# Kernel tuning notes

Hardware: AMD Instinct MI355X
Metric: run time of the kernel (lower is better)

## Reference

```python
import jax, jax.numpy as jnp
import numpy as np

NUM_GRAPHS = 64


def _gcn_conv(x, src, dst, W, b, n_nodes):
    # PyG GCNConv: add self-loops, symmetric degree normalization, scatter-add.
    s = jnp.concatenate([src, jnp.arange(n_nodes, dtype=src.dtype)])
    d = jnp.concatenate([dst, jnp.arange(n_nodes, dtype=dst.dtype)])
    deg = jax.ops.segment_sum(jnp.ones_like(d, dtype=x.dtype), d, num_segments=n_nodes)
    dinv = jnp.where(deg > 0, jax.lax.rsqrt(deg), 0.0)
    h = x @ W  # transform before gather: [N, H]
    msg = (dinv[s] * dinv[d])[:, None] * h[s]  # [E+N, H]
    out = jax.ops.segment_sum(msg, d, num_segments=n_nodes)
    return out + b


def reference(x, edge_index, batch, W1, b1, W2, b2, fcW1, fcb1, fcW2, fcb2):
    n_nodes = x.shape[0]
    src, dst = edge_index[0], edge_index[1]
    h = jax.nn.relu(_gcn_conv(x, src, dst, W1, b1, n_nodes))
    # dropout(p=0.5, training=False) is identity at inference
    h = jax.nn.relu(_gcn_conv(h, src, dst, W2, b2, n_nodes))
    # global_mean_pool over graph ids
    sums = jax.ops.segment_sum(h, batch, num_segments=NUM_GRAPHS)
    cnts = jax.ops.segment_sum(jnp.ones((n_nodes,), dtype=h.dtype), batch, num_segments=NUM_GRAPHS)
    g = sums / jnp.maximum(cnts, 1.0)[:, None]  # [G, H]
    g = jax.nn.relu(g @ fcW1 + fcb1)
    logits = g @ fcW2 + fcb2
    return jax.nn.log_softmax(logits, axis=1)


def setup_inputs() -> dict:
    key = jax.random.key(0)
    ks = jax.random.split(key, 8)
    N, E, D, H, C = 100000, 1600000, 128, 128, 10
    x = jax.random.normal(ks[0], (N, D), dtype=jnp.float32)
    edge_index = jax.random.randint(ks[1], (2, E), 0, N, dtype=jnp.int32)
    batch = jnp.sort(jax.random.randint(ks[2], (N,), 0, NUM_GRAPHS, dtype=jnp.int32))
    def w(k, fan_in, shape):
        return jax.random.normal(k, shape, dtype=jnp.float32) / np.sqrt(fan_in)
    return {
        'x': x, 'edge_index': edge_index, 'batch': batch,
        'W1': w(ks[3], D, (D, H)), 'b1': jnp.zeros((H,), jnp.float32),
        'W2': w(ks[4], H, (H, H)), 'b2': jnp.zeros((H,), jnp.float32),
        'fcW1': w(ks[5], H, (H, H)), 'fcb1': jnp.zeros((H,), jnp.float32),
        'fcW2': w(ks[6], H, (H, C)), 'fcb2': jnp.zeros((C,), jnp.float32),
    }
```

## Files before the change

kernel.cpp:

```cpp
#include <hip/hip_runtime.h>
#include <stdint.h>

#define TB 256

__device__ __forceinline__ float blo(uint32_t v) { return __uint_as_float(v << 16); }
__device__ __forceinline__ float bhi(uint32_t v) { return __uint_as_float(v & 0xffff0000u); }
__device__ __forceinline__ uint32_t f2b(float f) {
    uint32_t u = __float_as_uint(f);
    return (u + 0x7fffu + ((u >> 16) & 1u)) >> 16;
}
__device__ __forceinline__ uint32_t pack2(float lo, float hi) {
    return f2b(lo) | (f2b(hi) << 16);
}

__global__ void zero_u32(uint32_t* __restrict__ p, int n) {
    int i = blockIdx.x * blockDim.x + threadIdx.x;
    if (i < n) p[i] = 0u;
}

__global__ void hist_kernel(const int* __restrict__ dst, int E, int* __restrict__ cnt) {
    int e = blockIdx.x * blockDim.x + threadIdx.x;
    if (e < E) atomicAdd(&cnt[dst[e]], 1);
}

__global__ void dinv_kernel(const int* __restrict__ cnt, float* __restrict__ dinv, int N) {
    int n = blockIdx.x * blockDim.x + threadIdx.x;
    if (n < N) dinv[n] = rsqrtf((float)cnt[n] + 1.0f);
}

__global__ __launch_bounds__(256) void scan1_kernel(const int* __restrict__ cnt, int N,
                                                    int* __restrict__ rp, int* __restrict__ bsum) {
    __shared__ int sh[256];
    int t = threadIdx.x;
    int base = blockIdx.x * 1024 + t * 4;
    int v0 = (base + 0 < N) ? cnt[base + 0] : 0;
    int v1 = (base + 1 < N) ? cnt[base + 1] : 0;
    int v2 = (base + 2 < N) ? cnt[base + 2] : 0;
    int v3 = (base + 3 < N) ? cnt[base + 3] : 0;
    int s = v0 + v1 + v2 + v3;
    sh[t] = s;
    __syncthreads();
    for (int off = 1; off < 256; off <<= 1) {
        int add = (t >= off) ? sh[t - off] : 0;
        __syncthreads();
        sh[t] += add;
        __syncthreads();
    }
    int incl = sh[t];
    if (t == 255) bsum[blockIdx.x] = incl;
    int run = incl - s;
    if (base + 0 < N) rp[base + 0] = run; run += v0;
    if (base + 1 < N) rp[base + 1] = run; run += v1;
    if (base + 2 < N) rp[base + 2] = run; run += v2;
    if (base + 3 < N) rp[base + 3] = run;
}

__global__ __launch_bounds__(256) void scan2_kernel(int* __restrict__ bsum, int nblk) {
    __shared__ int sh[256];
    int t = threadIdx.x;
    int v = (t < nblk) ? bsum[t] : 0;
    sh[t] = v;
    __syncthreads();
    for (int off = 1; off < 256; off <<= 1) {
        int add = (t >= off) ? sh[t - off] : 0;
        __syncthreads();
        sh[t] += add;
        __syncthreads();
    }
    if (t < nblk) bsum[t] = sh[t] - v;
}

__global__ void scan3_kernel(int* __restrict__ rp, int* __restrict__ rfill,
                             const int* __restrict__ bsum, int N, int E) {
    int i = blockIdx.x * blockDim.x + threadIdx.x;
    if (i < N) {
        int v = rp[i] + bsum[i >> 10];
        rp[i] = v;
        rfill[i] = v;
    }
    if (i == 0) rp[N] = E;
}

__global__ void fill_kernel(const int* __restrict__ src, const int* __restrict__ dst, int E,
                            int* __restrict__ rfill, int2* __restrict__ edges,
                            const float* __restrict__ dinv) {
    int e = blockIdx.x * blockDim.x + threadIdx.x;
    if (e < E) {
        int s = src[e], d = dst[e];
        int pos = atomicAdd(&rfill[d], 1);
        int2 pr;
        pr.x = s;
        pr.y = __float_as_int(dinv[s] * dinv[d]);
        edges[pos] = pr;
    }
}

template <bool BF16IN>
__global__ __launch_bounds__(256) void gemm128_kernel(const void* __restrict__ Xv,
                                                      const float* __restrict__ W,
                                                      uint32_t* __restrict__ Y,
                                                      int N, int ntiles) {
    __shared__ float Ws[128 * 128];
    for (int i = threadIdx.x; i < 128 * 128 / 4; i += 256)
        ((float4*)Ws)[i] = ((const float4*)W)[i];
    __syncthreads();

    int tf = threadIdx.x & 31;
    int tn = threadIdx.x >> 5;
    int f0 = tf * 4;
    int j0 = tn * 4;

    for (int tile = blockIdx.x; tile < ntiles; tile += gridDim.x) {
        int n0 = tile * 32;
        int nn0 = min(n0 + j0 + 0, N - 1);
        int nn1 = min(n0 + j0 + 1, N - 1);
        int nn2 = min(n0 + j0 + 2, N - 1);
        int nn3 = min(n0 + j0 + 3, N - 1);
        float4 a0 = {0, 0, 0, 0}, a1 = {0, 0, 0, 0}, a2 = {0, 0, 0, 0}, a3 = {0, 0, 0, 0};

        if (BF16IN) {
            const uint16_t* xr0 = (const uint16_t*)Xv + (size_t)nn0 * 128;
            const uint16_t* xr1 = (const uint16_t*)Xv + (size_t)nn1 * 128;
            const uint16_t* xr2 = (const uint16_t*)Xv + (size_t)nn2 * 128;
            const uint16_t* xr3 = (const uint16_t*)Xv + (size_t)nn3 * 128;
#pragma unroll 4
            for (int k = 0; k < 128; k += 2) {
                float4 w0 = *(const float4*)(Ws + k * 128 + f0);
                float4 w1 = *(const float4*)(Ws + (k + 1) * 128 + f0);
                uint32_t u0 = *(const uint32_t*)(xr0 + k);
                uint32_t u1 = *(const uint32_t*)(xr1 + k);
                uint32_t u2 = *(const uint32_t*)(xr2 + k);
                uint32_t u3 = *(const uint32_t*)(xr3 + k);
                float x;
                x = blo(u0);
                a0.x = fmaf(x, w0.x, a0.x); a0.y = fmaf(x, w0.y, a0.y);
                a0.z = fmaf(x, w0.z, a0.z); a0.w = fmaf(x, w0.w, a0.w);
                x = bhi(u0);
                a0.x = fmaf(x, w1.x, a0.x); a0.y = fmaf(x, w1.y, a0.y);
                a0.z = fmaf(x, w1.z, a0.z); a0.w = fmaf(x, w1.w, a0.w);
                x = blo(u1);
                a1.x = fmaf(x, w0.x, a1.x); a1.y = fmaf(x, w0.y, a1.y);
                a1.z = fmaf(x, w0.z, a1.z); a1.w = fmaf(x, w0.w, a1.w);
                x = bhi(u1);
                a1.x = fmaf(x, w1.x, a1.x); a1.y = fmaf(x, w1.y, a1.y);
                a1.z = fmaf(x, w1.z, a1.z); a1.w = fmaf(x, w1.w, a1.w);
                x = blo(u2);
                a2.x = fmaf(x, w0.x, a2.x); a2.y = fmaf(x, w0.y, a2.y);
                a2.z = fmaf(x, w0.z, a2.z); a2.w = fmaf(x, w0.w, a2.w);
                x = bhi(u2);
                a2.x = fmaf(x, w1.x, a2.x); a2.y = fmaf(x, w1.y, a2.y);
                a2.z = fmaf(x, w1.z, a2.z); a2.w = fmaf(x, w1.w, a2.w);
                x = blo(u3);
                a3.x = fmaf(x, w0.x, a3.x); a3.y = fmaf(x, w0.y, a3.y);
                a3.z = fmaf(x, w0.z, a3.z); a3.w = fmaf(x, w0.w, a3.w);
                x = bhi(u3);
                a3.x = fmaf(x, w1.x, a3.x); a3.y = fmaf(x, w1.y, a3.y);
                a3.z = fmaf(x, w1.z, a3.z); a3.w = fmaf(x, w1.w, a3.w);
            }
        } else {
            const float* xr0 = (const float*)Xv + (size_t)nn0 * 128;
            const float* xr1 = (const float*)Xv + (size_t)nn1 * 128;
            const float* xr2 = (const float*)Xv + (size_t)nn2 * 128;
            const float* xr3 = (const float*)Xv + (size_t)nn3 * 128;
#pragma unroll 8
            for (int k = 0; k < 128; ++k) {
                float4 wv = *(const float4*)(Ws + k * 128 + f0);
                float x0 = xr0[k], x1 = xr1[k], x2 = xr2[k], x3 = xr3[k];
                a0.x = fmaf(x0, wv.x, a0.x); a0.y = fmaf(x0, wv.y, a0.y);
                a0.z = fmaf(x0, wv.z, a0.z); a0.w = fmaf(x0, wv.w, a0.w);
                a1.x = fmaf(x1, wv.x, a1.x); a1.y = fmaf(x1, wv.y, a1.y);
                a1.z = fmaf(x1, wv.z, a1.z); a1.w = fmaf(x1, wv.w, a1.w);
                a2.x = fmaf(x2, wv.x, a2.x); a2.y = fmaf(x2, wv.y, a2.y);
                a2.z = fmaf(x2, wv.z, a2.z); a2.w = fmaf(x2, wv.w, a2.w);
                a3.x = fmaf(x3, wv.x, a3.x); a3.y = fmaf(x3, wv.y, a3.y);
                a3.z = fmaf(x3, wv.z, a3.z); a3.w = fmaf(x3, wv.w, a3.w);
            }
        }
        int n;
        n = n0 + j0 + 0;
        if (n < N) { uint2 o = {pack2(a0.x, a0.y), pack2(a0.z, a0.w)};
                     *(uint2*)(Y + (size_t)n * 64 + tf * 2) = o; }
        n = n0 + j0 + 1;
        if (n < N) { uint2 o = {pack2(a1.x, a1.y), pack2(a1.z, a1.w)};
                     *(uint2*)(Y + (size_t)n * 64 + tf * 2) = o; }
        n = n0 + j0 + 2;
        if (n < N) { uint2 o = {pack2(a2.x, a2.y), pack2(a2.z, a2.w)};
                     *(uint2*)(Y + (size_t)n * 64 + tf * 2) = o; }
        n = n0 + j0 + 3;
        if (n < N) { uint2 o = {pack2(a3.x, a3.y), pack2(a3.z, a3.w)};
                     *(uint2*)(Y + (size_t)n * 64 + tf * 2) = o; }
    }
}

__global__ __launch_bounds__(256) void conv_kernel(const uint32_t* __restrict__ T,
                                                   const int* __restrict__ rp,
                                                   const int2* __restrict__ edges,
                                                   const float* __restrict__ dinv,
                                                   const float* __restrict__ bias,
                                                   uint32_t* __restrict__ OUT, int N) {
    int wid = (blockIdx.x * TB + threadIdx.x) >> 6;
    int lane = threadIdx.x & 63;
    if (wid >= N) return;
    int d = wid;
    float dv = dinv[d];
    uint32_t td = T[(size_t)d * 64 + lane];
    float accx = dv * dv * blo(td);
    float accy = dv * dv * bhi(td);
    int e0 = rp[d], e1 = rp[d + 1];
#pragma unroll 4
    for (int e = e0; e < e1; ++e) {
        int2 pr = edges[e];
        float w = __int_as_float(pr.y);
        uint32_t tv = T[(size_t)pr.x * 64 + lane];
        accx = fmaf(w, blo(tv), accx);
        accy = fmaf(w, bhi(tv), accy);
    }
    float2 b = *(const float2*)(bias + lane * 2);
    OUT[(size_t)d * 64 + lane] = pack2(fmaxf(accx + b.x, 0.0f), fmaxf(accy + b.y, 0.0f));
}

#define NPB 256
__global__ __launch_bounds__(128) void pool_kernel(const uint16_t* __restrict__ Hh,
                                                   const int* __restrict__ batch, int N,
                                                   float* __restrict__ gsum, int* __restrict__ gcnt) {
    int f = threadIdx.x;
    int n0 = blockIdx.x * NPB;
    if (n0 >= N) return;
    int n1 = min(n0 + NPB, N);
    int cur = batch[n0];
    float acc = 0.0f;
    int c = 0;
    for (int n = n0; n < n1; ++n) {
        int b = batch[n];
        if (b != cur) {
            atomicAdd(&gsum[cur * 128 + f], acc);
            if (f == 0) atomicAdd(&gcnt[cur], c);
            acc = 0.0f; c = 0; cur = b;
        }
        acc += __uint_as_float(((uint32_t)Hh[(size_t)n * 128 + f]) << 16);
        c++;
    }
    atomicAdd(&gsum[cur * 128 + f], acc);
    if (f == 0) atomicAdd(&gcnt[cur], c);
}

__global__ __launch_bounds__(128) void head_kernel(const float* __restrict__ gsum,
                                                   const int* __restrict__ gcnt,
                                                   const float* __restrict__ fcW1,
                                                   const float* __restrict__ fcb1,
                                                   const float* __restrict__ fcW2,
                                                   const float* __restrict__ fcb2,
                                                   float* __restrict__ out) {
    __shared__ float gx[128], hid[128], lg[10];
    int g = blockIdx.x, t = threadIdx.x;
    float cntf = fmaxf((float)gcnt[g], 1.0f);
    gx[t] = gsum[g * 128 + t] / cntf;
    __syncthreads();
    float a = fcb1[t];
    for (int k = 0; k < 128; ++k) a = fmaf(gx[k], fcW1[k * 128 + t], a);
    hid[t] = fmaxf(a, 0.0f);
    __syncthreads();
    if (t < 10) {
        float a2 = fcb2[t];
        for (int k = 0; k < 128; ++k) a2 = fmaf(hid[k], fcW2[k * 10 + t], a2);
        lg[t] = a2;
    }
    __syncthreads();
    if (t < 10) {
        float m = -1e30f;
        for (int j = 0; j < 10; ++j) m = fmaxf(m, lg[j]);
        float se = 0.0f;
        for (int j = 0; j < 10; ++j) se += expf(lg[j] - m);
        out[g * 10 + t] = lg[t] - m - logf(se);
    }
}

extern "C" void kernel_launch(void* const* d_in, const int* in_sizes, int n_in,
                              void* d_out, int out_size, void* d_ws, size_t ws_size,
                              hipStream_t stream) {
    const float* x    = (const float*)d_in[0];
    const int*   ei   = (const int*)d_in[1];
    const int*   batch= (const int*)d_in[2];
    const float* W1   = (const float*)d_in[3];
    const float* b1   = (const float*)d_in[4];
    const float* W2   = (const float*)d_in[5];
    const float* b2   = (const float*)d_in[6];
    const float* fcW1 = (const float*)d_in[7];
    const float* fcb1 = (const float*)d_in[8];
    const float* fcW2 = (const float*)d_in[9];
    const float* fcb2 = (const float*)d_in[10];
    float* out = (float*)d_out;

    int N = in_sizes[0] / 128;
    int E = in_sizes[1] / 2;
    const int* src = ei;
    const int* dst = ei + E;

    char* basep = (char*)d_ws;
    size_t off = 0;
    auto alloc = [&](size_t bytes) -> void* {
        off = (off + 255) & ~(size_t)255;
        void* p = basep + off;
        off += bytes;
        return p;
    };
    float*     dinv  = (float*)alloc((size_t)N * 4);
    int*       cnt   = (int*)alloc((size_t)N * 4);
    int*       rp    = (int*)alloc((size_t)(N + 1) * 4);
    int*       rfill = (int*)alloc((size_t)N * 4);
    int*       bsum  = (int*)alloc(1024 * 4);
    int2*      edges = (int2*)alloc((size_t)E * 8);
    uint32_t*  A     = (uint32_t*)alloc((size_t)N * 128 * 2);
    uint32_t*  B     = (uint32_t*)alloc((size_t)N * 128 * 2);
    float*     gsum  = (float*)alloc(64 * 128 * 4);
    int*       gcnt  = (int*)alloc(64 * 4);

    int nblk = (N + 1023) / 1024;
    int ntiles = (N + 31) / 32;

    zero_u32<<<(N + TB - 1) / TB, TB, 0, stream>>>((uint32_t*)cnt, N);
    hist_kernel<<<(E + TB - 1) / TB, TB, 0, stream>>>(dst, E, cnt);
    dinv_kernel<<<(N + TB - 1) / TB, TB, 0, stream>>>(cnt, dinv, N);

    scan1_kernel<<<nblk, 256, 0, stream>>>(cnt, N, rp, bsum);
    scan2_kernel<<<1, 256, 0, stream>>>(bsum, nblk);
    scan3_kernel<<<(N + TB - 1) / TB, TB, 0, stream>>>(rp, rfill, bsum, N, E);
    fill_kernel<<<(E + TB - 1) / TB, TB, 0, stream>>>(src, dst, E, rfill, edges, dinv);

    gemm128_kernel<false><<<1024, 256, 0, stream>>>(x, W1, A, N, ntiles);
    conv_kernel<<<(N + 3) / 4, TB, 0, stream>>>(A, rp, edges, dinv, b1, B, N);

    gemm128_kernel<true><<<1024, 256, 0, stream>>>(B, W2, A, N, ntiles);
    conv_kernel<<<(N + 3) / 4, TB, 0, stream>>>(A, rp, edges, dinv, b2, B, N);

    zero_u32<<<(64 * 128 + TB - 1) / TB, TB, 0, stream>>>((uint32_t*)gsum, 64 * 128);
    zero_u32<<<1, 64, 0, stream>>>((uint32_t*)gcnt, 64);
    pool_kernel<<<(N + NPB - 1) / NPB, 128, 0, stream>>>((const uint16_t*)B, batch, N, gsum, gcnt);

    head_kernel<<<64, 128, 0, stream>>>(gsum, gcnt, fcW1, fcb1, fcW2, fcb2, out);
}
```

Baseline: 628.1 us.

## Replace scalar FMA node-transform GEMM with bf16 MFMA kernel

Replaces the FP32 FMA-based 128x128 GEMM with a kernel using MFMA 16x16x32 bf16 instructions. Weights are converted to bf16 and stored transposed in padded shared memory, then held in registers as B fragments. The fp32 input for layer one is rounded to bf16 before the multiply, which adds precision loss in exchange for higher matrix throughput. Output is written as scattered 16-bit stores.

```diff
diff --git a/kernel.cpp b/kernel.cpp
--- a/kernel.cpp
+++ b/kernel.cpp
@@ -2,6 +2,9 @@
 #include <stdint.h>
 
 #define TB 256
+
+typedef short short8 __attribute__((ext_vector_type(8)));
+typedef float f32x4 __attribute__((ext_vector_type(4)));
 
 __device__ __forceinline__ float blo(uint32_t v) { return __uint_as_float(v << 16); }
 __device__ __forceinline__ float bhi(uint32_t v) { return __uint_as_float(v & 0xffff0000u); }
@@ -96,99 +99,81 @@
 }
 
 template <bool BF16IN>
-__global__ __launch_bounds__(256) void gemm128_kernel(const void* __restrict__ Xv,
-                                                      const float* __restrict__ W,
-                                                      uint32_t* __restrict__ Y,
-                                                      int N, int ntiles) {
-    __shared__ float Ws[128 * 128];
-    for (int i = threadIdx.x; i < 128 * 128 / 4; i += 256)
-        ((float4*)Ws)[i] = ((const float4*)W)[i];
-    __syncthreads();
-
-    int tf = threadIdx.x & 31;
-    int tn = threadIdx.x >> 5;
-    int f0 = tf * 4;
-    int j0 = tn * 4;
+__global__ __launch_bounds__(256) void gemm_mfma_kernel(const void* __restrict__ Xv,
+                                                        const float* __restrict__ W,
+                                                        uint16_t* __restrict__ Y,
+                                                        int N, int ntiles) {
+    __shared__ uint16_t Wb[128][136];
+
+    for (int idx = threadIdx.x; idx < 128 * 32; idx += 256) {
+        int k = idx >> 5;
+        int c4 = (idx & 31) * 4;
+        float4 wv = *(const float4*)(W + (size_t)k * 128 + c4);
+        Wb[c4 + 0][k] = (uint16_t)f2b(wv.x);
+        Wb[c4 + 1][k] = (uint16_t)f2b(wv.y);
+        Wb[c4 + 2][k] = (uint16_t)f2b(wv.z);
+        Wb[c4 + 3][k] = (uint16_t)f2b(wv.w);
+    }
+    __syncthreads();
+
+    int w = threadIdx.x >> 6;
+    int l = threadIdx.x & 63;
+    int rowOff = (w & 1) * 16;
+    int colBase = (w >> 1) * 64;
+    int lr = l & 15;
+    int k8 = (l >> 4) * 8;
+
+    short8 bfrag[4][4];
+#pragma unroll
+    for (int ct = 0; ct < 4; ++ct)
+#pragma unroll
+        for (int kk = 0; kk < 4; ++kk)
+            bfrag[ct][kk] = *(const short8*)&Wb[colBase + ct * 16 + lr][kk * 32 + k8];
 
     for (int tile = blockIdx.x; tile < ntiles; tile += gridDim.x) {
-        int n0 = tile * 32;
-        int nn0 = min(n0 + j0 + 0, N - 1);
-        int nn1 = min(n0 + j0 + 1, N - 1);
-        int nn2 = min(n0 + j0 + 2, N - 1);
-        int nn3 = min(n0 + j0 + 3, N - 1);
-        float4 a0 = {0, 0, 0, 0}, a1 = {0, 0, 0, 0}, a2 = {0, 0, 0, 0}, a3 = {0, 0, 0, 0};
-
+        int rbase = tile * 32 + rowOff;
+        int r = min(rbase + lr, N - 1);
+
+        short8 afrag[4];
         if (BF16IN) {
-            const uint16_t* xr0 = (const uint16_t*)Xv + (size_t)nn0 * 128;
-            const uint16_t* xr1 = (const uint16_t*)Xv + (size_t)nn1 * 128;
-            const uint16_t* xr2 = (const uint16_t*)Xv + (size_t)nn2 * 128;
-            const uint16_t* xr3 = (const uint16_t*)Xv + (size_t)nn3 * 128;
-#pragma unroll 4
-            for (int k = 0; k < 128; k += 2) {
-                float4 w0 = *(const float4*)(Ws + k * 128 + f0);
-                float4 w1 = *(const float4*)(Ws + (k + 1) * 128 + f0);
-                uint32_t u0 = *(const uint32_t*)(xr0 + k);
-                uint32_t u1 = *(const uint32_t*)(xr1 + k);
-                uint32_t u2 = *(const uint32_t*)(xr2 + k);
-                uint32_t u3 = *(const uint32_t*)(xr3 + k);
-                float x;
-                x = blo(u0);
-                a0.x = fmaf(x, w0.x, a0.x); a0.y = fmaf(x, w0.y, a0.y);
-                a0.z = fmaf(x, w0.z, a0.z); a0.w = fmaf(x, w0.w, a0.w);
-                x = bhi(u0);
-                a0.x = fmaf(x, w1.x, a0.x); a0.y = fmaf(x, w1.y, a0.y);
-                a0.z = fmaf(x, w1.z, a0.z); a0.w = fmaf(x, w1.w, a0.w);
-                x = blo(u1);
-                a1.x = fmaf(x, w0.x, a1.x); a1.y = fmaf(x, w0.y, a1.y);
-                a1.z = fmaf(x, w0.z, a1.z); a1.w = fmaf(x, w0.w, a1.w);
-                x = bhi(u1);
-                a1.x = fmaf(x, w1.x, a1.x); a1.y = fmaf(x, w1.y, a1.y);
-                a1.z = fmaf(x, w1.z, a1.z); a1.w = fmaf(x, w1.w, a1.w);
-                x = blo(u2);
-                a2.x = fmaf(x, w0.x, a2.x); a2.y = fmaf(x, w0.y, a2.y);
-                a2.z = fmaf(x, w0.z, a2.z); a2.w = fmaf(x, w0.w, a2.w);
-                x = bhi(u2);
-                a2.x = fmaf(x, w1.x, a2.x); a2.y = fmaf(x, w1.y, a2.y);
-                a2.z = fmaf(x, w1.z, a2.z); a2.w = fmaf(x, w1.w, a2.w);
-                x = blo(u3);
-                a3.x = fmaf(x, w0.x, a3.x); a3.y = fmaf(x, w0.y, a3.y);
-                a3.z = fmaf(x, w0.z, a3.z); a3.w = fmaf(x, w0.w, a3.w);
-                x = bhi(u3);
-                a3.x = fmaf(x, w1.x, a3.x); a3.y = fmaf(x, w1.y, a3.y);
-                a3.z = fmaf(x, w1.z, a3.z); a3.w = fmaf(x, w1.w, a3.w);
-            }
+            const uint16_t* xr = (const uint16_t*)Xv + (size_t)r * 128 + k8;
+#pragma unroll
+            for (int kk = 0; kk < 4; ++kk)
+                afrag[kk] = *(const short8*)(xr + kk * 32);
         } else {
-            const float* xr0 = (const float*)Xv + (size_t)nn0 * 128;
-            const float* xr1 = (const float*)Xv + (size_t)nn1 * 128;
-            const float* xr2 = (const float*)Xv + (size_t)nn2 * 128;
-            const float* xr3 = (const float*)Xv + (size_t)nn3 * 128;
-#pragma unroll 8
-            for (int k = 0; k < 128; ++k) {
-                float4 wv = *(const float4*)(Ws + k * 128 + f0);
-                float x0 = xr0[k], x1 = xr1[k], x2 = xr2[k], x3 = xr3[k];
-                a0.x = fmaf(x0, wv.x, a0.x); a0.y = fmaf(x0, wv.y, a0.y);
-                a0.z = fmaf(x0, wv.z, a0.z); a0.w = fmaf(x0, wv.w, a0.w);
-                a1.x = fmaf(x1, wv.x, a1.x); a1.y = fmaf(x1, wv.y, a1.y);
-                a1.z = fmaf(x1, wv.z, a1.z); a1.w = fmaf(x1, wv.w, a1.w);
-                a2.x = fmaf(x2, wv.x, a2.x); a2.y = fmaf(x2, wv.y, a2.y);
-                a2.z = fmaf(x2, wv.z, a2.z); a2.w = fmaf(x2, wv.w, a2.w);
-                a3.x = fmaf(x3, wv.x, a3.x); a3.y = fmaf(x3, wv.y, a3.y);
-                a3.z = fmaf(x3, wv.z, a3.z); a3.w = fmaf(x3, wv.w, a3.w);
+            const float* xr = (const float*)Xv + (size_t)r * 128 + k8;
+#pragma unroll
+            for (int kk = 0; kk < 4; ++kk) {
+                float4 f0 = *(const float4*)(xr + kk * 32);
+                float4 f1 = *(const float4*)(xr + kk * 32 + 4);
+                short8 a;
+                a[0] = (short)f2b(f0.x); a[1] = (short)f2b(f0.y);
+                a[2] = (short)f2b(f0.z); a[3] = (short)f2b(f0.w);
+                a[4] = (short)f2b(f1.x); a[5] = (short)f2b(f1.y);
+                a[6] = (short)f2b(f1.z); a[7] = (short)f2b(f1.w);
+                afrag[kk] = a;
             }
         }
-        int n;
-        n = n0 + j0 + 0;
-        if (n < N) { uint2 o = {pack2(a0.x, a0.y), pack2(a0.z, a0.w)};
-                     *(uint2*)(Y + (size_t)n * 64 + tf * 2) = o; }
-        n = n0 + j0 + 1;
-        if (n < N) { uint2 o = {pack2(a1.x, a1.y), pack2(a1.z, a1.w)};
-                     *(uint2*)(Y + (size_t)n * 64 + tf * 2) = o; }
-        n = n0 + j0 + 2;
-        if (n < N) { uint2 o = {pack2(a2.x, a2.y), pack2(a2.z, a2.w)};
-                     *(uint2*)(Y + (size_t)n * 64 + tf * 2) = o; }
-        n = n0 + j0 + 3;
-        if (n < N) { uint2 o = {pack2(a3.x, a3.y), pack2(a3.z, a3.w)};
-                     *(uint2*)(Y + (size_t)n * 64 + tf * 2) = o; }
+
+        f32x4 acc[4] = {{0, 0, 0, 0}, {0, 0, 0, 0}, {0, 0, 0, 0}, {0, 0, 0, 0}};
+#pragma unroll
+        for (int kk = 0; kk < 4; ++kk)
+#pragma unroll
+            for (int ct = 0; ct < 4; ++ct)
+                acc[ct] = __builtin_amdgcn_mfma_f32_16x16x32_bf16(afrag[kk], bfrag[ct][kk],
+                                                                  acc[ct], 0, 0, 0);
+
+        int rs = rbase + (l >> 4) * 4;
+#pragma unroll
+        for (int i = 0; i < 4; ++i) {
+            int rr = rs + i;
+            if (rr < N) {
+                uint16_t* yr = Y + (size_t)rr * 128 + colBase + lr;
+#pragma unroll
+                for (int ct = 0; ct < 4; ++ct)
+                    yr[ct * 16] = (uint16_t)f2b(acc[ct][i]);
+            }
+        }
     }
 }
 
@@ -327,10 +312,10 @@
     scan3_kernel<<<(N + TB - 1) / TB, TB, 0, stream>>>(rp, rfill, bsum, N, E);
     fill_kernel<<<(E + TB - 1) / TB, TB, 0, stream>>>(src, dst, E, rfill, edges, dinv);
 
-    gemm128_kernel<false><<<1024, 256, 0, stream>>>(x, W1, A, N, ntiles);
+    gemm_mfma_kernel<false><<<1024, 256, 0, stream>>>(x, W1, (uint16_t*)A, N, ntiles);
     conv_kernel<<<(N + 3) / 4, TB, 0, stream>>>(A, rp, edges, dinv, b1, B, N);
 
-    gemm128_kernel<true><<<1024, 256, 0, stream>>>(B, W2, A, N, ntiles);
+    gemm_mfma_kernel<true><<<1024, 256, 0, stream>>>(B, W2, (uint16_t*)A, N, ntiles);
     conv_kernel<<<(N + 3) / 4, TB, 0, stream>>>(A, rp, edges, dinv, b2, B, N);
 
     zero_u32<<<(64 * 128 + TB - 1) / TB, TB, 0, stream>>>((uint32_t*)gsum, 64 * 128);
```

New measurement: 537.2 us. 1.17x faster.
